# Kernel tuning notes

Measured on AMD Instinct MI355X. Metric: run time of the kernel, lower is better.

The kernel has to match this reference:

```python
import jax, jax.numpy as jnp
import numpy as np

K = 15
P_DIM = 3
C_IN = 64
C_OUT = 64
KP_EXTENT = 0.06
RADIUS = 0.1
B, N, NNEIGHB = 1, 50000, 32


def _make_kernel_points(key):
    # Stand-in for load_kernels: K points in a sphere of given radius, first at center.
    pts = jax.random.normal(key, (K, P_DIM), dtype=jnp.float32)
    pts = pts / (jnp.linalg.norm(pts, axis=1, keepdims=True) + 1e-6)
    r = jax.random.uniform(jax.random.fold_in(key, 1), (K, 1), dtype=jnp.float32) ** (1.0 / P_DIM)
    pts = pts * r * RADIUS
    pts = pts.at[0].set(0.0)  # fixed 'center' point
    return pts


def setup_inputs() -> dict:
    key = jax.random.key(0)
    k1, k2, k3, k4, k5, k6, k7 = jax.random.split(key, 7)
    q_pts = jax.random.uniform(k1, (B, N, P_DIM), dtype=jnp.float32)
    s_pts = jax.random.uniform(k2, (B, 60000, P_DIM), dtype=jnp.float32)
    # neighbor coordinates near the query points (within conv radius)
    neighbors = q_pts[:, :, None, :] + (jax.random.uniform(k3, (B, N, NNEIGHB, P_DIM), dtype=jnp.float32) - 0.5) * (2 * RADIUS)
    neighb_inds = jax.random.randint(k4, (B, N, NNEIGHB), 0, 60000, dtype=jnp.int64)
    x = jax.random.normal(k5, (B, N, NNEIGHB, C_IN), dtype=jnp.float32)
    kernel_points = _make_kernel_points(k6)
    # kaiming_uniform_(a=sqrt(5)) on [K, C_in, C_out]: bound = sqrt(6/((1+5)*fan_in)), fan_in = C_in
    bound = float(np.sqrt(6.0 / (6.0 * C_IN)))
    weights = jax.random.uniform(k7, (K, C_IN, C_OUT), minval=-bound, maxval=bound, dtype=jnp.float32)
    return {"q_pts": q_pts, "s_pts": s_pts, "neighbors": neighbors,
            "neighb_inds": neighb_inds, "x": x,
            "kernel_points": kernel_points, "weights": weights}


def reference(q_pts, s_pts, neighbors, neighb_inds, x, kernel_points, weights):
    # Center neighbor coordinates on query points: [B,N,n,3]
    rel = neighbors - q_pts[:, :, None, :]
    # Differences to kernel points: [B,N,n,K,3]
    diff = rel[:, :, :, None, :] - kernel_points[None, None, None, :, :]
    sq_distances = jnp.sum(diff * diff, axis=-1)  # [B,N,n,K]
    # Linear influence, clamped at 0, transposed to [B,N,K,n]
    all_weights = jnp.clip(1.0 - jnp.sqrt(sq_distances) / KP_EXTENT, 0.0, None)
    all_weights = jnp.swapaxes(all_weights, -2, -1)
    # Weighted neighbor features per kernel point: [B,N,K,Cin]
    weighted = jnp.einsum('bnkm,bnmc->bnkc', all_weights, x)
    # Per-kernel-point matmul with weights [K,Cin,Cout], summed over K: [B,N,Cout]
    out = jnp.einsum('bnkc,kcd->bnd', weighted, weights)
    return out
```

## Files before the change

### kernel.cpp

```cpp
#include <hip/hip_runtime.h>


typedef __attribute__((ext_vector_type(8))) short bf16x8;
typedef __attribute__((ext_vector_type(4))) float f32x4;

#define NPTS        50000
#define PTS_PER_WG  16
#define KP_INV      (1.0f / 0.06f)

static __device__ __forceinline__ short f2bf(float f) {
    union { float f; unsigned u; } v; v.f = f;
    unsigned r = v.u + 0x7fffu + ((v.u >> 16) & 1u);
    return (short)(r >> 16);
}

__launch_bounds__(256, 4)
__global__ void kpconv_kernel(const float* __restrict__ q_pts,
                              const float* __restrict__ neighbors,
                              const float* __restrict__ x,
                              const float* __restrict__ kp,
                              const float* __restrict__ weights,
                              float* __restrict__ out) {
    __shared__ __align__(16) unsigned short wa[4][640];
    __shared__ __align__(16) unsigned short A2[PTS_PER_WG * 1024];

    const int tid   = threadIdx.x;
    const int wv    = tid >> 6;
    const int lane  = tid & 63;
    const int quad  = lane >> 4;
    const int r16   = lane & 15;
    const int wg    = blockIdx.x;

    const int m32   = lane & 31;
    const int khalf = lane >> 5;

    for (int i = 0; i < 4; ++i) {
        const int  p = wv * 4 + i;
        const long n = (long)wg * PTS_PER_WG + p;

        const float qx = q_pts[n*3 + 0];
        const float qy = q_pts[n*3 + 1];
        const float qz = q_pts[n*3 + 2];
        const float rx = neighbors[n*96 + m32*3 + 0] - qx;
        const float ry = neighbors[n*96 + m32*3 + 1] - qy;
        const float rz = neighbors[n*96 + m32*3 + 2] - qz;
        #pragma unroll
        for (int kk = 0; kk < 8; ++kk) {
            const int k  = kk * 2 + khalf;
            const int kc = (k < 15) ? k : 14;
            const float dx = rx - kp[kc*3 + 0];
            const float dy = ry - kp[kc*3 + 1];
            const float dz = rz - kp[kc*3 + 2];
            float w = 1.0f - sqrtf(dx*dx + dy*dy + dz*dz) * KP_INV;
            w = (k < 15) ? fmaxf(w, 0.0f) : 0.0f;
            wa[wv][k*40 + m32] = (unsigned short)f2bf(w);
        }
        __syncthreads();

        const bf16x8 af = *(const bf16x8*)&wa[wv][r16*40 + quad*8];

        const float* xp = x + n*2048 + (long)quad*512;
        #pragma unroll
        for (int t = 0; t < 4; ++t) {
            const int c = t*16 + r16;
            bf16x8 bf;
            #pragma unroll
            for (int j = 0; j < 8; ++j) bf[j] = f2bf(xp[c + j*64]);
            f32x4 acc = {0.f, 0.f, 0.f, 0.f};
            acc = __builtin_amdgcn_mfma_f32_16x16x32_bf16(af, bf, acc, 0, 0, 0);
            #pragma unroll
            for (int reg = 0; reg < 4; ++reg) {
                const int k  = quad*4 + reg;
                const int k2 = k*64 + c;
                const int ch = k2 >> 3;
                A2[p*1024 + ((ch ^ (p & 7)) << 3) + (k2 & 7)]
                    = (unsigned short)f2bf(acc[reg]);
            }
        }
    }

    __syncthreads();

    const int d = wv*16 + r16;
    f32x4 oacc = {0.f, 0.f, 0.f, 0.f};
    for (int kk = 0; kk < 30; ++kk) {
        const int ch = kk*4 + quad;
        const bf16x8 a2 = *(const bf16x8*)&A2[r16*1024 + ((ch ^ (r16 & 7)) << 3)];
        const float* wp = weights + (kk*32 + quad*8)*64 + d;
        bf16x8 bw;
        #pragma unroll
        for (int j = 0; j < 8; ++j) bw[j] = f2bf(wp[j*64]);
        oacc = __builtin_amdgcn_mfma_f32_16x16x32_bf16(a2, bw, oacc, 0, 0, 0);
    }

    #pragma unroll
    for (int reg = 0; reg < 4; ++reg) {
        const int p = quad*4 + reg;
        out[((long)wg * PTS_PER_WG + p)*64 + d] = oacc[reg];
    }
}

extern "C" void kernel_launch(void* const* d_in, const int* in_sizes, int n_in,
                              void* d_out, int out_size, void* d_ws, size_t ws_size,
                              hipStream_t stream) {
    const float* q_pts     = (const float*)d_in[0];
    const float* neighbors = (const float*)d_in[2];
    const float* x         = (const float*)d_in[4];
    const float* kp        = (const float*)d_in[5];
    const float* weights   = (const float*)d_in[6];
    float* out = (float*)d_out;

    dim3 grid(NPTS / PTS_PER_WG);
    kpconv_kernel<<<grid, 256, 0, stream>>>(q_pts, neighbors, x, kp, weights, out);
}
```

Before: 572.4 us.

## Vectorize x loads, transpose via LDS, prepack bf16 weights in workspace

Loads x with coalesced float4 reads, converts it to bf16 in LDS, and uses ds_read_b64_tr_b16 transposed reads to build MFMA operands instead of strided scalar loads. Swaps the MFMA operand order so the intermediate can be stored as short4 into a smaller swizzled A2 buffer. A separate prep kernel packs the weights into bf16 in the workspace so the second GEMM does one 16-byte load per step. It also hoists kernel-point loads, drops the per-point syncthreads, and lowers the occupancy hint to 3. This costs an extra kernel launch and more LDS and registers per block.

```diff
diff --git a/kernel.cpp b/kernel.cpp
--- a/kernel.cpp
+++ b/kernel.cpp
@@ -2,27 +2,36 @@
 
 
 typedef __attribute__((ext_vector_type(8))) short bf16x8;
+typedef __attribute__((ext_vector_type(4))) short short4v;
 typedef __attribute__((ext_vector_type(4))) float f32x4;
 
 #define NPTS        50000
 #define PTS_PER_WG  16
 #define KP_INV      (1.0f / 0.06f)
+#define WP_ELEMS    (120 * 64 * 8)
 
-static __device__ __forceinline__ short f2bf(float f) {
-    union { float f; unsigned u; } v; v.f = f;
-    unsigned r = v.u + 0x7fffu + ((v.u >> 16) & 1u);
-    return (short)(r >> 16);
+static __device__ __forceinline__ short fbf(float f) {
+    union { __bf16 h; short s; } u; u.h = (__bf16)f; return u.s;
 }
 
-__launch_bounds__(256, 4)
+__global__ void prep_weights(const float* __restrict__ w, unsigned short* __restrict__ wp) {
+    const int ch = blockIdx.x;
+    const int t  = threadIdx.x;
+    const int d  = t >> 3, j = t & 7;
+    wp[(ch * 64 + d) * 8 + j] = (unsigned short)fbf(w[(ch * 8 + j) * 64 + d]);
+}
+
+__launch_bounds__(256, 3)
 __global__ void kpconv_kernel(const float* __restrict__ q_pts,
                               const float* __restrict__ neighbors,
                               const float* __restrict__ x,
                               const float* __restrict__ kp,
                               const float* __restrict__ weights,
+                              const unsigned short* __restrict__ wp,
                               float* __restrict__ out) {
     __shared__ __align__(16) unsigned short wa[4][640];
-    __shared__ __align__(16) unsigned short A2[PTS_PER_WG * 1024];
+    __shared__ __align__(16) unsigned short xs[4][2048];
+    __shared__ __align__(16) unsigned short A2[PTS_PER_WG * 960];
 
     const int tid   = threadIdx.x;
     const int wv    = tid >> 6;
@@ -34,69 +43,112 @@
     const int m32   = lane & 31;
     const int khalf = lane >> 5;
 
+    float kpx[8], kpy[8], kpz[8];
+    #pragma unroll
+    for (int kk = 0; kk < 8; ++kk) {
+        const int k  = kk * 2 + khalf;
+        const int kc = (k < 15) ? k : 14;
+        kpx[kk] = kp[kc * 3 + 0];
+        kpy[kk] = kp[kc * 3 + 1];
+        kpz[kk] = kp[kc * 3 + 2];
+    }
+
+    const int xwb = ((lane >> 2) & 3) * 64 + (lane >> 4) * 16 + (lane & 3) * 4;
+    const unsigned xsbase = (unsigned)(unsigned long long)(&xs[wv][0]);
+    const unsigned xa = xsbase + (unsigned)(quad * 1024 + r16 * 8);
+
     for (int i = 0; i < 4; ++i) {
         const int  p = wv * 4 + i;
         const long n = (long)wg * PTS_PER_WG + p;
 
-        const float qx = q_pts[n*3 + 0];
-        const float qy = q_pts[n*3 + 1];
-        const float qz = q_pts[n*3 + 2];
-        const float rx = neighbors[n*96 + m32*3 + 0] - qx;
-        const float ry = neighbors[n*96 + m32*3 + 1] - qy;
-        const float rz = neighbors[n*96 + m32*3 + 2] - qz;
+        const float4* xsrc = (const float4*)(x + n * 2048) + lane;
+        float4 xr[8];
+        #pragma unroll
+        for (int it = 0; it < 8; ++it) xr[it] = xsrc[it * 64];
+
+        const float qx = q_pts[n * 3 + 0];
+        const float qy = q_pts[n * 3 + 1];
+        const float qz = q_pts[n * 3 + 2];
+        const float rx = neighbors[n * 96 + m32 * 3 + 0] - qx;
+        const float ry = neighbors[n * 96 + m32 * 3 + 1] - qy;
+        const float rz = neighbors[n * 96 + m32 * 3 + 2] - qz;
         #pragma unroll
         for (int kk = 0; kk < 8; ++kk) {
-            const int k  = kk * 2 + khalf;
-            const int kc = (k < 15) ? k : 14;
-            const float dx = rx - kp[kc*3 + 0];
-            const float dy = ry - kp[kc*3 + 1];
-            const float dz = rz - kp[kc*3 + 2];
-            float w = 1.0f - sqrtf(dx*dx + dy*dy + dz*dz) * KP_INV;
+            const int k = kk * 2 + khalf;
+            const float dx = rx - kpx[kk];
+            const float dy = ry - kpy[kk];
+            const float dz = rz - kpz[kk];
+            float w = 1.0f - sqrtf(dx * dx + dy * dy + dz * dz) * KP_INV;
             w = (k < 15) ? fmaxf(w, 0.0f) : 0.0f;
-            wa[wv][k*40 + m32] = (unsigned short)f2bf(w);
+            wa[wv][k * 40 + m32] = (unsigned short)fbf(w);
         }
-        __syncthreads();
 
-        const bf16x8 af = *(const bf16x8*)&wa[wv][r16*40 + quad*8];
+        const bf16x8 wf = *(const bf16x8*)&wa[wv][r16 * 40 + quad * 8];
 
-        const float* xp = x + n*2048 + (long)quad*512;
+        #pragma unroll
+        for (int it = 0; it < 8; ++it) {
+            short4v sv = { fbf(xr[it].x), fbf(xr[it].y), fbf(xr[it].z), fbf(xr[it].w) };
+            *(short4v*)&xs[wv][it * 256 + xwb] = sv;
+        }
+
+        short4v t0, t1, t2, t3, t4, t5, t6, t7;
+        asm volatile("ds_read_b64_tr_b16 %0, %1"            : "=v"(t0) : "v"(xa) : "memory");
+        asm volatile("ds_read_b64_tr_b16 %0, %1 offset:512" : "=v"(t1) : "v"(xa) : "memory");
+        asm volatile("ds_read_b64_tr_b16 %0, %1 offset:128" : "=v"(t2) : "v"(xa) : "memory");
+        asm volatile("ds_read_b64_tr_b16 %0, %1 offset:640" : "=v"(t3) : "v"(xa) : "memory");
+        asm volatile("ds_read_b64_tr_b16 %0, %1 offset:256" : "=v"(t4) : "v"(xa) : "memory");
+        asm volatile("ds_read_b64_tr_b16 %0, %1 offset:768" : "=v"(t5) : "v"(xa) : "memory");
+        asm volatile("ds_read_b64_tr_b16 %0, %1 offset:384" : "=v"(t6) : "v"(xa) : "memory");
+        asm volatile("ds_read_b64_tr_b16 %0, %1 offset:896" : "=v"(t7) : "v"(xa) : "memory");
+        asm volatile("s_waitcnt lgkmcnt(0)" ::: "memory");
+        __builtin_amdgcn_sched_barrier(0);
+
         #pragma unroll
         for (int t = 0; t < 4; ++t) {
-            const int c = t*16 + r16;
-            bf16x8 bf;
-            #pragma unroll
-            for (int j = 0; j < 8; ++j) bf[j] = f2bf(xp[c + j*64]);
+            const short4v lo = (t == 0) ? t0 : (t == 1) ? t2 : (t == 2) ? t4 : t6;
+            const short4v hi = (t == 0) ? t1 : (t == 1) ? t3 : (t == 2) ? t5 : t7;
+            const bf16x8 xf = __builtin_shufflevector(lo, hi, 0, 1, 2, 3, 4, 5, 6, 7);
             f32x4 acc = {0.f, 0.f, 0.f, 0.f};
-            acc = __builtin_amdgcn_mfma_f32_16x16x32_bf16(af, bf, acc, 0, 0, 0);
-            #pragma unroll
-            for (int reg = 0; reg < 4; ++reg) {
-                const int k  = quad*4 + reg;
-                const int k2 = k*64 + c;
-                const int ch = k2 >> 3;
-                A2[p*1024 + ((ch ^ (p & 7)) << 3) + (k2 & 7)]
-                    = (unsigned short)f2bf(acc[reg]);
+            acc = __builtin_amdgcn_mfma_f32_16x16x32_bf16(xf, wf, acc, 0, 0, 0);
+            if (r16 < 15) {
+                const int ch  = r16 * 8 + t * 2 + (quad >> 1);
+                const int sig = ch ^ ((p ^ r16) & 7);
+                short4v ov = { fbf(acc[0]), fbf(acc[1]), fbf(acc[2]), fbf(acc[3]) };
+                *(short4v*)&A2[p * 960 + sig * 8 + (quad & 1) * 4] = ov;
             }
         }
     }
 
     __syncthreads();
 
-    const int d = wv*16 + r16;
+    const int d = wv * 16 + r16;
     f32x4 oacc = {0.f, 0.f, 0.f, 0.f};
-    for (int kk = 0; kk < 30; ++kk) {
-        const int ch = kk*4 + quad;
-        const bf16x8 a2 = *(const bf16x8*)&A2[r16*1024 + ((ch ^ (r16 & 7)) << 3)];
-        const float* wp = weights + (kk*32 + quad*8)*64 + d;
-        bf16x8 bw;
-        #pragma unroll
-        for (int j = 0; j < 8; ++j) bw[j] = f2bf(wp[j*64]);
-        oacc = __builtin_amdgcn_mfma_f32_16x16x32_bf16(a2, bw, oacc, 0, 0, 0);
+    if (wp) {
+        #pragma unroll 2
+        for (int kk = 0; kk < 30; ++kk) {
+            const int ch  = kk * 4 + quad;
+            const int sig = ch ^ ((r16 ^ (ch >> 3)) & 7);
+            const bf16x8 a2 = *(const bf16x8*)&A2[r16 * 960 + sig * 8];
+            const bf16x8 bw = *(const bf16x8*)(wp + (ch * 64 + d) * 8);
+            oacc = __builtin_amdgcn_mfma_f32_16x16x32_bf16(a2, bw, oacc, 0, 0, 0);
+        }
+    } else {
+        for (int kk = 0; kk < 30; ++kk) {
+            const int ch  = kk * 4 + quad;
+            const int sig = ch ^ ((r16 ^ (ch >> 3)) & 7);
+            const bf16x8 a2 = *(const bf16x8*)&A2[r16 * 960 + sig * 8];
+            const float* wsrc = weights + (kk * 32 + quad * 8) * 64 + d;
+            bf16x8 bw;
+            #pragma unroll
+            for (int j = 0; j < 8; ++j) bw[j] = fbf(wsrc[j * 64]);
+            oacc = __builtin_amdgcn_mfma_f32_16x16x32_bf16(a2, bw, oacc, 0, 0, 0);
+        }
     }
 
     #pragma unroll
     for (int reg = 0; reg < 4; ++reg) {
-        const int p = quad*4 + reg;
-        out[((long)wg * PTS_PER_WG + p)*64 + d] = oacc[reg];
+        const int pp = quad * 4 + reg;
+        out[((long)wg * PTS_PER_WG + pp) * 64 + d] = oacc[reg];
     }
 }
 
@@ -110,6 +162,10 @@
     const float* weights   = (const float*)d_in[6];
     float* out = (float*)d_out;
 
+    unsigned short* wp = (d_ws && ws_size >= (size_t)(WP_ELEMS * 2))
+                       ? (unsigned short*)d_ws : nullptr;
+    if (wp) prep_weights<<<dim3(120), dim3(512), 0, stream>>>(weights, wp);
+
     dim3 grid(NPTS / PTS_PER_WG);
-    kpconv_kernel<<<grid, 256, 0, stream>>>(q_pts, neighbors, x, kp, weights, out);
+    kpconv_kernel<<<grid, 256, 0, stream>>>(q_pts, neighbors, x, kp, weights, wp, out);
 }
```

New measurement: 557.1 us. 2.7% less time.
